# Performance work log

Hardware: AMD Instinct MI355X
Metric: run time of the kernel (lower is better)

Reference implementation:

```python
import jax, jax.numpy as jnp
import numpy as np

N_NODES = 100000
IN_DIM, HID_DIM, OUT_DIM = 1433, 16, 7
N_EDGES = 3200000


def gcn_conv(x, edge_index, W, b, num_nodes):
    # add self loops
    loop = jnp.arange(num_nodes, dtype=edge_index.dtype)
    src = jnp.concatenate([edge_index[0], loop])  # [E+N]
    dst = jnp.concatenate([edge_index[1], loop])
    h = x @ W + b  # [N, out]
    # degree computed on row (edge_index[0]) as in the torch code
    deg = jax.ops.segment_sum(jnp.ones_like(src, dtype=h.dtype), src,
                              num_segments=num_nodes)
    dis = deg ** -0.5  # self-loops guarantee deg >= 1
    norm = dis[src] * dis[dst]  # [E+N]
    msg = norm[:, None] * h[src]  # gather + scale
    return jax.ops.segment_sum(msg, dst, num_segments=num_nodes)  # scatter-add


def setup_inputs() -> dict:
    key = jax.random.key(0)
    k1, k2, k3, k4, k5, k6 = jax.random.split(key, 6)
    x = jax.random.normal(k1, (N_NODES, IN_DIM), dtype=jnp.float32)
    edge_index = jax.random.randint(k2, (2, N_EDGES), 0, N_NODES, dtype=jnp.int64)
    s1 = 1.0 / np.sqrt(IN_DIM)
    s2 = 1.0 / np.sqrt(HID_DIM)
    W1 = jax.random.uniform(k3, (IN_DIM, HID_DIM), jnp.float32, -s1, s1)
    b1 = jax.random.uniform(k4, (HID_DIM,), jnp.float32, -s1, s1)
    W2 = jax.random.uniform(k5, (HID_DIM, OUT_DIM), jnp.float32, -s2, s2)
    b2 = jax.random.uniform(k6, (OUT_DIM,), jnp.float32, -s2, s2)
    return {"x": x, "edge_index": edge_index, "W1": W1, "b1": b1,
            "W2": W2, "b2": b2}


def reference(x, edge_index, W1, b1, W2, b2):
    n = x.shape[0]
    h = gcn_conv(x, edge_index, W1, b1, n)
    h = jax.nn.relu(h)
    # dropout is inactive in eval mode (training=False)
    h = gcn_conv(h, edge_index, W2, b2, n)
    return jax.nn.log_softmax(h, axis=1)
```

## Files before the change

kernel.cpp:

```cpp
#include <hip/hip_runtime.h>
#include <math.h>

constexpr int IN_DIM = 1433;
constexpr int HID    = 16;
constexpr int OUTD   = 7;

__device__ __forceinline__ int edge_get(const int* __restrict__ ei, long long idx, int is64) {
    return is64 ? ei[2 * idx] : ei[idx];
}

__global__ void k_detect(const int* __restrict__ ei, int* __restrict__ flag) {
    __shared__ int nzsh;
    if (threadIdx.x == 0) nzsh = 0;
    __syncthreads();
    int nz = 0;
    for (int i = threadIdx.x; i < 2048; i += blockDim.x)
        nz |= (ei[2 * i + 1] != 0) ? 1 : 0;
    if (nz) nzsh = 1;
    __syncthreads();
    if (threadIdx.x == 0) *flag = (nzsh == 0) ? 1 : 0;
}

__global__ void k_init_new(int* __restrict__ deg, int* __restrict__ cnt, int n) {
    int i = blockIdx.x * blockDim.x + threadIdx.x;
    if (i < n) { deg[i] = 1; cnt[i] = 0; }
}

__global__ void k_deg_finish(float* __restrict__ dis, int n) {
    int i = blockIdx.x * blockDim.x + threadIdx.x;
    if (i < n) {
        int v = ((const int*)dis)[i];
        dis[i] = rsqrtf((float)v);
    }
}

__global__ __launch_bounds__(128) void k_gemm1h(
        const float* __restrict__ x, const float* __restrict__ W1,
        const float* __restrict__ b1, float* __restrict__ h1, int n,
        const int* __restrict__ ei, int E, const int* __restrict__ flag,
        int* __restrict__ deg, int* __restrict__ cnt, int nHist) {
    if ((int)blockIdx.x < nHist) {
        int is64 = *flag;
        long long stride = (long long)nHist * blockDim.x;
        for (long long e = (long long)blockIdx.x * blockDim.x + threadIdx.x;
             e < E; e += stride) {
            int s = edge_get(ei, e, is64);
            int d = edge_get(ei, (long long)E + e, is64);
            atomicAdd(&deg[s], 1);
            atomicAdd(&cnt[d], 1);
        }
        return;
    }

    constexpr int BK = 32, XST = 36;
    __shared__ __align__(16) float xs[128 * XST];
    __shared__ __align__(16) float wsm[BK * HID];
    const int t    = threadIdx.x;
    const int c4   = t & 3;
    const int rq   = t >> 2;
    const int row0 = ((int)blockIdx.x - nHist) * 128;

    float xreg[32];
    float wreg[4];
    float acc[16];
    #pragma unroll
    for (int j = 0; j < 16; ++j) acc[j] = 0.f;

    auto issue = [&](int kt) {
        #pragma unroll
        for (int i = 0; i < 32; ++i) {
            int idx  = t + 128 * i;
            int srow = idx >> 5;
            int scol = idx & 31;
            int gr   = row0 + srow;
            int col  = kt + scol;
            float v = 0.f;
            if (gr < n && col < IN_DIM) v = x[(long long)gr * IN_DIM + col];
            xreg[i] = v;
        }
        #pragma unroll
        for (int u = 0; u < 4; ++u) {
            int idx = t + 128 * u;
            int kk  = idx >> 4;
            wreg[u] = (kt + kk < IN_DIM) ? W1[(kt + kk) * HID + (idx & 15)] : 0.f;
        }
    };
    auto commit = [&]() {
        #pragma unroll
        for (int i = 0; i < 32; ++i) {
            int idx  = t + 128 * i;
            int srow = idx >> 5;
            int scol = idx & 31;
            xs[srow * XST + scol] = xreg[i];
        }
        #pragma unroll
        for (int u = 0; u < 4; ++u) wsm[t + 128 * u] = wreg[u];
    };

    const int nkt = (IN_DIM + BK - 1) / BK;
    issue(0);
    for (int it = 0; it < nkt; ++it) {
        commit();
        __syncthreads();
        if (it + 1 < nkt) issue((it + 1) * BK);
        #pragma unroll 8
        for (int k = 0; k < BK; ++k) {
            float4 w = *(const float4*)&wsm[k * HID + c4 * 4];
            #pragma unroll
            for (int j = 0; j < 4; ++j) {
                float xv = xs[(rq + 32 * j) * XST + k];
                acc[j * 4 + 0] += xv * w.x;
                acc[j * 4 + 1] += xv * w.y;
                acc[j * 4 + 2] += xv * w.z;
                acc[j * 4 + 3] += xv * w.w;
            }
        }
        __syncthreads();
    }

    float4 bv = *(const float4*)&b1[c4 * 4];
    #pragma unroll
    for (int j = 0; j < 4; ++j) {
        int gr = row0 + rq + 32 * j;
        if (gr < n) {
            float4 hv;
            hv.x = acc[j * 4 + 0] + bv.x;
            hv.y = acc[j * 4 + 1] + bv.y;
            hv.z = acc[j * 4 + 2] + bv.z;
            hv.w = acc[j * 4 + 3] + bv.w;
            *(float4*)&h1[(long long)gr * HID + c4 * 4] = hv;
        }
    }
}

__global__ void k_scale(const float* __restrict__ dis, const float* __restrict__ in,
                        float* __restrict__ out, int n, int squared) {
    int i = blockIdx.x * blockDim.x + threadIdx.x;
    if (i >= n * 4) return;
    int row = i >> 2;
    float d = dis[row];
    if (squared) d *= d;
    float4 v = *(const float4*)&in[(long long)i * 4];
    v.x *= d; v.y *= d; v.z *= d; v.w *= d;
    *(float4*)&out[(long long)i * 4] = v;
}

__global__ __launch_bounds__(256) void k_scan1(const int* __restrict__ cnt,
                                               int* __restrict__ bsum, int n) {
    __shared__ int sh[256];
    int t = threadIdx.x;
    int base = blockIdx.x * 1024 + t * 4;
    int s = 0;
    #pragma unroll
    for (int j = 0; j < 4; ++j) {
        int i = base + j;
        if (i < n) s += cnt[i];
    }
    sh[t] = s; __syncthreads();
    for (int o = 128; o > 0; o >>= 1) {
        if (t < o) sh[t] += sh[t + o];
        __syncthreads();
    }
    if (t == 0) bsum[blockIdx.x] = sh[0];
}

__global__ __launch_bounds__(256) void k_scan2(const int* __restrict__ bsum,
                                               int* __restrict__ boff,
                                               int* __restrict__ rp,
                                               int nb, int n, int E) {
    __shared__ int sh[256];
    int t = threadIdx.x;
    int v = (t < nb) ? bsum[t] : 0;
    sh[t] = v; __syncthreads();
    for (int o = 1; o < 256; o <<= 1) {
        int tmp = (t >= o) ? sh[t - o] : 0;
        __syncthreads();
        sh[t] += tmp;
        __syncthreads();
    }
    boff[t] = sh[t] - v;
    if (t == 0) rp[n] = E;
}

__global__ __launch_bounds__(256) void k_scan3(const int* __restrict__ cnt,
                                               const int* __restrict__ boff,
                                               int* __restrict__ rp,
                                               int* __restrict__ cur, int n) {
    __shared__ int sh[256];
    int t = threadIdx.x;
    int base = blockIdx.x * 1024 + t * 4;
    int c[4];
    int s = 0;
    #pragma unroll
    for (int j = 0; j < 4; ++j) {
        int i = base + j;
        c[j] = (i < n) ? cnt[i] : 0;
        s += c[j];
    }
    sh[t] = s; __syncthreads();
    for (int o = 1; o < 256; o <<= 1) {
        int tmp = (t >= o) ? sh[t - o] : 0;
        __syncthreads();
        sh[t] += tmp;
        __syncthreads();
    }
    int run = boff[blockIdx.x] + sh[t] - s;
    #pragma unroll
    for (int j = 0; j < 4; ++j) {
        int i = base + j;
        if (i < n) { rp[i] = run; cur[i] = run; }
        run += c[j];
    }
}

__global__ void k_fill(const int* __restrict__ ei, int E, const int* __restrict__ flag,
                       int* __restrict__ cur, int* __restrict__ csr) {
    int e = blockIdx.x * blockDim.x + threadIdx.x;
    if (e >= E) return;
    int is64 = *flag;
    int s = edge_get(ei, e, is64);
    int d = edge_get(ei, (long long)E + e, is64);
    int slot = atomicAdd(&cur[d], 1);
    csr[slot] = s;
}

__global__ __launch_bounds__(256) void k_gather1f(
        const int* __restrict__ rp, const int* __restrict__ csr,
        const float* __restrict__ dis, const float* __restrict__ hs1,
        const float* __restrict__ W2, const float* __restrict__ b2,
        float* __restrict__ hs2, int n) {
    __shared__ float w2s[HID * OUTD];
    __shared__ float b2s[OUTD];
    int t = threadIdx.x;
    if (t < HID * OUTD) w2s[t] = W2[t];
    if (t < OUTD) b2s[t] = b2[t];
    __syncthreads();

    int tid  = blockIdx.x * blockDim.x + t;
    int node = tid >> 2;
    int q    = tid & 3;
    if (node >= n) return;

    float4 acc = *(const float4*)&hs1[(long long)node * HID + q * 4];

    int i = rp[node], end = rp[node + 1];
    if (i < end) {
        int    s1  = csr[i];
        float4 hv1 = *(const float4*)&hs1[(long long)s1 * HID + q * 4];
        for (++i; i < end; ++i) {
            int    s2  = csr[i];
            float4 hv2 = *(const float4*)&hs1[(long long)s2 * HID + q * 4];
            acc.x += hv1.x; acc.y += hv1.y; acc.z += hv1.z; acc.w += hv1.w;
            hv1 = hv2;
        }
        acc.x += hv1.x; acc.y += hv1.y; acc.z += hv1.z; acc.w += hv1.w;
    }

    float dn = dis[node];
    float r0 = fmaxf(dn * acc.x, 0.f), r1 = fmaxf(dn * acc.y, 0.f);
    float r2 = fmaxf(dn * acc.z, 0.f), r3 = fmaxf(dn * acc.w, 0.f);
    float p[OUTD];
    #pragma unroll
    for (int j = 0; j < OUTD; ++j) {
        p[j] = r0 * w2s[(q * 4 + 0) * OUTD + j]
             + r1 * w2s[(q * 4 + 1) * OUTD + j]
             + r2 * w2s[(q * 4 + 2) * OUTD + j]
             + r3 * w2s[(q * 4 + 3) * OUTD + j];
    }
    #pragma unroll
    for (int j = 0; j < OUTD; ++j) {
        p[j] += __shfl_xor(p[j], 1, 4);
        p[j] += __shfl_xor(p[j], 2, 4);
    }
    hs2[(long long)node * OUTD + q] = dn * (p[q] + b2s[q]);
    if (q < 3) hs2[(long long)node * OUTD + q + 4] = dn * (p[q + 4] + b2s[q + 4]);
}

__global__ __launch_bounds__(256) void k_gather2(
        const int* __restrict__ rp, const int* __restrict__ csr,
        const float* __restrict__ dis, const float* __restrict__ hs2,
        float* __restrict__ out, int n) {
    int t = threadIdx.x;
    int node = blockIdx.x * 32 + (t >> 3);
    int q = t & 7;
    if (node >= n) return;
    float acc = -1e30f;
    if (q < OUTD) {
        acc = hs2[(long long)node * OUTD + q];
        int i = rp[node], end = rp[node + 1];
        if (i < end) {
            int   s1 = csr[i];
            float v1 = hs2[(long long)s1 * OUTD + q];
            for (++i; i < end; ++i) {
                int   s2 = csr[i];
                float v2 = hs2[(long long)s2 * OUTD + q];
                acc += v1;
                v1 = v2;
            }
            acc += v1;
        }
        acc *= dis[node];
    }
    float m = acc;
    #pragma unroll
    for (int o = 1; o < 8; o <<= 1) m = fmaxf(m, __shfl_xor(m, o, 8));
    float ex = (q < OUTD) ? expf(acc - m) : 0.f;
    float ss = ex;
    #pragma unroll
    for (int o = 1; o < 8; o <<= 1) ss += __shfl_xor(ss, o, 8);
    if (q < OUTD) out[(long long)node * OUTD + q] = acc - m - logf(ss);
}

__global__ void k_deg_init(int* __restrict__ deg, int n) {
    int i = blockIdx.x * blockDim.x + threadIdx.x;
    if (i < n) deg[i] = 1;
}

__global__ void k_deg_count(const int* __restrict__ ei, int E,
                            const int* __restrict__ flag, int* __restrict__ deg) {
    int e = blockIdx.x * blockDim.x + threadIdx.x;
    if (e >= E) return;
    int is64 = *flag;
    int s = edge_get(ei, e, is64);
    atomicAdd(&deg[s], 1);
}

__global__ void k_agg1(const int* __restrict__ ei, int E, const int* __restrict__ flag,
                       const float* __restrict__ dis, const float* __restrict__ h1,
                       float* __restrict__ a1) {
    long long tid = (long long)blockIdx.x * blockDim.x + threadIdx.x;
    int e = (int)(tid >> 2);
    int q = (int)(tid & 3);
    if (e >= E) return;
    int is64 = *flag;
    int s = edge_get(ei, e, is64);
    int d = edge_get(ei, (long long)E + e, is64);
    float nrm = dis[s] * dis[d];
    float4 v = *(const float4*)&h1[(long long)s * HID + q * 4];
    float* o = &a1[(long long)d * HID + q * 4];
    atomicAdd(o + 0, nrm * v.x);
    atomicAdd(o + 1, nrm * v.y);
    atomicAdd(o + 2, nrm * v.z);
    atomicAdd(o + 3, nrm * v.w);
}

__global__ __launch_bounds__(256) void k_gemm2(
        const float* __restrict__ a1, const float* __restrict__ W2,
        const float* __restrict__ b2, const float* __restrict__ dis,
        float* __restrict__ h2, float* __restrict__ a2, int n) {
    __shared__ float w2s[HID * OUTD];
    __shared__ float b2s[OUTD];
    int t = threadIdx.x;
    if (t < HID * OUTD) w2s[t] = W2[t];
    if (t < OUTD) b2s[t] = b2[t];
    __syncthreads();
    int r = blockIdx.x * blockDim.x + t;
    if (r >= n) return;
    float a[16];
    #pragma unroll
    for (int i = 0; i < 4; ++i) {
        float4 v = *(const float4*)&a1[(long long)r * HID + i * 4];
        a[4 * i + 0] = fmaxf(v.x, 0.f);
        a[4 * i + 1] = fmaxf(v.y, 0.f);
        a[4 * i + 2] = fmaxf(v.z, 0.f);
        a[4 * i + 3] = fmaxf(v.w, 0.f);
    }
    float dd = 0.f;
    if (a2) { float d = dis[r]; dd = d * d; }
    #pragma unroll
    for (int j = 0; j < OUTD; ++j) {
        float acc = b2s[j];
        #pragma unroll
        for (int k = 0; k < HID; ++k) acc += a[k] * w2s[k * OUTD + j];
        h2[(long long)r * OUTD + j] = acc;
        if (a2) a2[(long long)r * OUTD + j] = dd * acc;
    }
}

__global__ void k_agg2(const int* __restrict__ ei, int E, const int* __restrict__ flag,
                       const float* __restrict__ dis, const float* __restrict__ h2,
                       float* __restrict__ a2) {
    long long tid = (long long)blockIdx.x * blockDim.x + threadIdx.x;
    int e = (int)(tid >> 1);
    int q = (int)(tid & 1);
    if (e >= E) return;
    int is64 = *flag;
    int s = edge_get(ei, e, is64);
    int d = edge_get(ei, (long long)E + e, is64);
    float nrm = dis[s] * dis[d];
    int cnt = q ? 3 : 4;
    long long bs = (long long)s * OUTD + q * 4;
    long long bd = (long long)d * OUTD + q * 4;
    #pragma unroll
    for (int j = 0; j < 4; ++j)
        if (j < cnt) atomicAdd(&a2[bd + j], nrm * h2[bs + j]);
}

__global__ void k_lsm(const float* __restrict__ a2, float* __restrict__ out, int n) {
    int r = blockIdx.x * blockDim.x + threadIdx.x;
    if (r >= n) return;
    float v[OUTD];
    #pragma unroll
    for (int j = 0; j < OUTD; ++j) v[j] = a2[(long long)r * OUTD + j];
    float m = v[0];
    #pragma unroll
    for (int j = 1; j < OUTD; ++j) m = fmaxf(m, v[j]);
    float ssum = 0.f;
    #pragma unroll
    for (int j = 0; j < OUTD; ++j) ssum += expf(v[j] - m);
    float l = logf(ssum);
    #pragma unroll
    for (int j = 0; j < OUTD; ++j) out[(long long)r * OUTD + j] = v[j] - m - l;
}

extern "C" void kernel_launch(void* const* d_in, const int* in_sizes, int n_in,
                              void* d_out, int out_size, void* d_ws, size_t ws_size,
                              hipStream_t stream) {
    const float* x  = (const float*)d_in[0];
    const int*   ei = (const int*)d_in[1];
    const float* W1 = (const float*)d_in[2];
    const float* b1 = (const float*)d_in[3];
    const float* W2 = (const float*)d_in[4];
    const float* b2 = (const float*)d_in[5];
    float* out = (float*)d_out;

    const int N = in_sizes[0] / IN_DIM;
    const int E = in_sizes[1] / 2;

    const int TPB = 256;
    const int gN  = (N + TPB - 1) / TPB;
    const int gE  = (E + TPB - 1) / TPB;
    const int gG1 = (N + 127) / 128;
    const int NB  = (N + 1023) / 1024;
    const int nHist = 512;

    float* ws = (float*)d_ws;
    size_t o = 0;
    auto take = [&](size_t cnt) { size_t r = o; o += (cnt + 127) & ~(size_t)127; return r; };

    size_t off_dis  = take((size_t)N);
    size_t off_flag = take(64);
    size_t off_cnt  = take((size_t)N);
    size_t off_rp   = take((size_t)N + 1);
    size_t off_cur  = take((size_t)N);
    size_t off_bs   = take(256);
    size_t off_bo   = take(256);
    size_t off_csr  = take((size_t)E);
    size_t off_h1   = take((size_t)N * HID);
    size_t off_h2   = take((size_t)N * OUTD);
    size_t need_new = o * sizeof(float);

    if (ws_size >= need_new) {
        float* dis  = ws + off_dis;
        int*   degi = (int*)dis;
        int*   flag = (int*)(ws + off_flag);
        int*   cnt  = (int*)(ws + off_cnt);
        int*   rp   = (int*)(ws + off_rp);
        int*   cur  = (int*)(ws + off_cur);
        int*   bs   = (int*)(ws + off_bs);
        int*   bo   = (int*)(ws + off_bo);
        int*   csr  = (int*)(ws + off_csr);
        float* h1   = ws + off_h1;
        float* hs2  = ws + off_h2;

        k_detect<<<1, 256, 0, stream>>>(ei, flag);
        k_init_new<<<gN, TPB, 0, stream>>>(degi, cnt, N);
        k_gemm1h<<<nHist + gG1, 128, 0, stream>>>(x, W1, b1, h1, N,
                                                  ei, E, flag, degi, cnt, nHist);
        k_deg_finish<<<gN, TPB, 0, stream>>>(dis, N);
        k_scan1<<<NB, 256, 0, stream>>>(cnt, bs, N);
        k_scan2<<<1, 256, 0, stream>>>(bs, bo, rp, NB, N, E);
        k_scan3<<<NB, 256, 0, stream>>>(cnt, bo, rp, cur, N);
        k_scale<<<(int)(((long long)N * 4 + TPB - 1) / TPB), TPB, 0, stream>>>(
            dis, h1, h1, N, 0);
        k_fill<<<gE, TPB, 0, stream>>>(ei, E, flag, cur, csr);
        k_gather1f<<<(int)(((long long)N * 4 + TPB - 1) / TPB), TPB, 0, stream>>>(
            rp, csr, dis, h1, W2, b2, hs2, N);
        k_gather2<<<(N + 31) / 32, 256, 0, stream>>>(rp, csr, dis, hs2, out, N);
    } else {
        o = 0;
        size_t f_dis  = take((size_t)N);
        size_t f_flag = take(64);
        size_t f_h1   = take((size_t)N * HID);
        size_t f_a1   = take((size_t)N * HID);
        size_t f_h2   = take((size_t)N * OUTD);
        size_t f_a2   = take((size_t)N * OUTD);

        float* dis  = ws + f_dis;
        int*   degi = (int*)dis;
        int*   flag = (int*)(ws + f_flag);
        float* h1   = ws + f_h1;
        float* a1   = ws + f_a1;
        float* h2   = ws + f_h2;
        float* a2   = ws + f_a2;

        int g4E = (int)(((long long)4 * E + TPB - 1) / TPB);
        int g2E = (int)(((long long)2 * E + TPB - 1) / TPB);

        k_detect<<<1, 256, 0, stream>>>(ei, flag);
        k_deg_init<<<gN, TPB, 0, stream>>>(degi, N);
        k_deg_count<<<gE, TPB, 0, stream>>>(ei, E, flag, degi);
        k_deg_finish<<<gN, TPB, 0, stream>>>(dis, N);
        k_gemm1h<<<gG1, 128, 0, stream>>>(x, W1, b1, h1, N,
                                          ei, E, flag, nullptr, nullptr, 0);
        k_scale<<<(int)(((long long)N * 4 + TPB - 1) / TPB), TPB, 0, stream>>>(
            dis, h1, a1, N, 1);
        k_agg1<<<g4E, TPB, 0, stream>>>(ei, E, flag, dis, h1, a1);
        k_gemm2<<<gN, TPB, 0, stream>>>(a1, W2, b2, dis, h2, a2, N);
        k_agg2<<<g2E, TPB, 0, stream>>>(ei, E, flag, dis, h2, a2);
        k_lsm<<<gN, TPB, 0, stream>>>(a2, out, N);
    }
}
```

Measured before the change: 776.4 us.

## Split histogram from GEMM, record per-edge slots, and unroll gathers

```diff
diff --git a/kernel.cpp b/kernel.cpp
--- a/kernel.cpp
+++ b/kernel.cpp
@@ -34,37 +34,115 @@
     }
 }
 
-__global__ __launch_bounds__(128) void k_gemm1h(
+__global__ void k_hist2(const int* __restrict__ ei, int E, const int* __restrict__ flag,
+                        int* __restrict__ deg, int* __restrict__ cnt,
+                        int* __restrict__ packed) {
+    int e = blockIdx.x * blockDim.x + threadIdx.x;
+    if (e >= E) return;
+    int is64 = *flag;
+    int s = edge_get(ei, e, is64);
+    int d = edge_get(ei, (long long)E + e, is64);
+    atomicAdd(&deg[s], 1);
+    int slot = atomicAdd(&cnt[d], 1);
+    packed[e] = (d << 14) | (slot & 16383);
+}
+
+__global__ void k_place(const int* __restrict__ ei, int E, const int* __restrict__ flag,
+                        const int* __restrict__ packed, const int* __restrict__ rp,
+                        int* __restrict__ csr) {
+    int e = blockIdx.x * blockDim.x + threadIdx.x;
+    if (e >= E) return;
+    int is64 = *flag;
+    int s  = edge_get(ei, e, is64);
+    int p  = packed[e];
+    int d  = p >> 14;
+    int sl = p & 16383;
+    csr[rp[d] + sl] = s;
+}
+
+__global__ __launch_bounds__(256) void k_scan1(const int* __restrict__ cnt,
+                                               int* __restrict__ bsum, int n) {
+    __shared__ int sh[256];
+    int t = threadIdx.x;
+    int base = blockIdx.x * 1024 + t * 4;
+    int s = 0;
+    #pragma unroll
+    for (int j = 0; j < 4; ++j) {
+        int i = base + j;
+        if (i < n) s += cnt[i];
+    }
+    sh[t] = s; __syncthreads();
+    for (int o = 128; o > 0; o >>= 1) {
+        if (t < o) sh[t] += sh[t + o];
+        __syncthreads();
+    }
+    if (t == 0) bsum[blockIdx.x] = sh[0];
+}
+
+__global__ __launch_bounds__(256) void k_scan2(const int* __restrict__ bsum,
+                                               int* __restrict__ boff,
+                                               int* __restrict__ rp,
+                                               int nb, int n, int E) {
+    __shared__ int sh[256];
+    int t = threadIdx.x;
+    int v = (t < nb) ? bsum[t] : 0;
+    sh[t] = v; __syncthreads();
+    for (int o = 1; o < 256; o <<= 1) {
+        int tmp = (t >= o) ? sh[t - o] : 0;
+        __syncthreads();
+        sh[t] += tmp;
+        __syncthreads();
+    }
+    boff[t] = sh[t] - v;
+    if (t == 0) rp[n] = E;
+}
+
+__global__ __launch_bounds__(256) void k_scan3(const int* __restrict__ cnt,
+                                               const int* __restrict__ boff,
+                                               int* __restrict__ rp, int n) {
+    __shared__ int sh[256];
+    int t = threadIdx.x;
+    int base = blockIdx.x * 1024 + t * 4;
+    int c[4];
+    int s = 0;
+    #pragma unroll
+    for (int j = 0; j < 4; ++j) {
+        int i = base + j;
+        c[j] = (i < n) ? cnt[i] : 0;
+        s += c[j];
+    }
+    sh[t] = s; __syncthreads();
+    for (int o = 1; o < 256; o <<= 1) {
+        int tmp = (t >= o) ? sh[t - o] : 0;
+        __syncthreads();
+        sh[t] += tmp;
+        __syncthreads();
+    }
+    int run = boff[blockIdx.x] + sh[t] - s;
+    #pragma unroll
+    for (int j = 0; j < 4; ++j) {
+        int i = base + j;
+        if (i < n) rp[i] = run;
+        run += c[j];
+    }
+}
+
+__global__ __launch_bounds__(128) void k_gemm1(
         const float* __restrict__ x, const float* __restrict__ W1,
-        const float* __restrict__ b1, float* __restrict__ h1, int n,
-        const int* __restrict__ ei, int E, const int* __restrict__ flag,
-        int* __restrict__ deg, int* __restrict__ cnt, int nHist) {
-    if ((int)blockIdx.x < nHist) {
-        int is64 = *flag;
-        long long stride = (long long)nHist * blockDim.x;
-        for (long long e = (long long)blockIdx.x * blockDim.x + threadIdx.x;
-             e < E; e += stride) {
-            int s = edge_get(ei, e, is64);
-            int d = edge_get(ei, (long long)E + e, is64);
-            atomicAdd(&deg[s], 1);
-            atomicAdd(&cnt[d], 1);
-        }
-        return;
-    }
-
+        const float* __restrict__ b1, float* __restrict__ h1, int n) {
     constexpr int BK = 32, XST = 36;
     __shared__ __align__(16) float xs[128 * XST];
     __shared__ __align__(16) float wsm[BK * HID];
     const int t    = threadIdx.x;
     const int c4   = t & 3;
     const int rq   = t >> 2;
-    const int row0 = ((int)blockIdx.x - nHist) * 128;
+    const int row0 = blockIdx.x * 128;
 
     float xreg[32];
     float wreg[4];
-    float acc[16];
-    #pragma unroll
-    for (int j = 0; j < 16; ++j) acc[j] = 0.f;
+    float4 acc[4];
+    #pragma unroll
+    for (int j = 0; j < 4; ++j) acc[j] = make_float4(0.f, 0.f, 0.f, 0.f);
 
     auto issue = [&](int kt) {
         #pragma unroll
@@ -103,16 +181,20 @@
         commit();
         __syncthreads();
         if (it + 1 < nkt) issue((it + 1) * BK);
-        #pragma unroll 8
-        for (int k = 0; k < BK; ++k) {
-            float4 w = *(const float4*)&wsm[k * HID + c4 * 4];
+        #pragma unroll
+        for (int k4 = 0; k4 < BK / 4; ++k4) {
+            int k = k4 * 4;
+            float4 w0 = *(const float4*)&wsm[(k + 0) * HID + c4 * 4];
+            float4 w1 = *(const float4*)&wsm[(k + 1) * HID + c4 * 4];
+            float4 w2 = *(const float4*)&wsm[(k + 2) * HID + c4 * 4];
+            float4 w3 = *(const float4*)&wsm[(k + 3) * HID + c4 * 4];
             #pragma unroll
             for (int j = 0; j < 4; ++j) {
-                float xv = xs[(rq + 32 * j) * XST + k];
-                acc[j * 4 + 0] += xv * w.x;
-                acc[j * 4 + 1] += xv * w.y;
-                acc[j * 4 + 2] += xv * w.z;
-                acc[j * 4 + 3] += xv * w.w;
+                float4 xv = *(const float4*)&xs[(rq + 32 * j) * XST + k];
+                acc[j].x += xv.x * w0.x + xv.y * w1.x + xv.z * w2.x + xv.w * w3.x;
+                acc[j].y += xv.x * w0.y + xv.y * w1.y + xv.z * w2.y + xv.w * w3.y;
+                acc[j].z += xv.x * w0.z + xv.y * w1.z + xv.z * w2.z + xv.w * w3.z;
+                acc[j].w += xv.x * w0.w + xv.y * w1.w + xv.z * w2.w + xv.w * w3.w;
             }
         }
         __syncthreads();
@@ -124,10 +206,10 @@
         int gr = row0 + rq + 32 * j;
         if (gr < n) {
             float4 hv;
-            hv.x = acc[j * 4 + 0] + bv.x;
-            hv.y = acc[j * 4 + 1] + bv.y;
-            hv.z = acc[j * 4 + 2] + bv.z;
-            hv.w = acc[j * 4 + 3] + bv.w;
+            hv.x = acc[j].x + bv.x;
+            hv.y = acc[j].y + bv.y;
+            hv.z = acc[j].z + bv.z;
+            hv.w = acc[j].w + bv.w;
             *(float4*)&h1[(long long)gr * HID + c4 * 4] = hv;
         }
     }
@@ -143,85 +225,6 @@
     float4 v = *(const float4*)&in[(long long)i * 4];
     v.x *= d; v.y *= d; v.z *= d; v.w *= d;
     *(float4*)&out[(long long)i * 4] = v;
-}
-
-__global__ __launch_bounds__(256) void k_scan1(const int* __restrict__ cnt,
-                                               int* __restrict__ bsum, int n) {
-    __shared__ int sh[256];
-    int t = threadIdx.x;
-    int base = blockIdx.x * 1024 + t * 4;
-    int s = 0;
-    #pragma unroll
-    for (int j = 0; j < 4; ++j) {
-        int i = base + j;
-        if (i < n) s += cnt[i];
-    }
-    sh[t] = s; __syncthreads();
-    for (int o = 128; o > 0; o >>= 1) {
-        if (t < o) sh[t] += sh[t + o];
-        __syncthreads();
-    }
-    if (t == 0) bsum[blockIdx.x] = sh[0];
-}
-
-__global__ __launch_bounds__(256) void k_scan2(const int* __restrict__ bsum,
-                                               int* __restrict__ boff,
-                                               int* __restrict__ rp,
-                                               int nb, int n, int E) {
-    __shared__ int sh[256];
-    int t = threadIdx.x;
-    int v = (t < nb) ? bsum[t] : 0;
-    sh[t] = v; __syncthreads();
-    for (int o = 1; o < 256; o <<= 1) {
-        int tmp = (t >= o) ? sh[t - o] : 0;
-        __syncthreads();
-        sh[t] += tmp;
-        __syncthreads();
-    }
-    boff[t] = sh[t] - v;
-    if (t == 0) rp[n] = E;
-}
-
-__global__ __launch_bounds__(256) void k_scan3(const int* __restrict__ cnt,
-                                               const int* __restrict__ boff,
-                                               int* __restrict__ rp,
-                                               int* __restrict__ cur, int n) {
-    __shared__ int sh[256];
-    int t = threadIdx.x;
-    int base = blockIdx.x * 1024 + t * 4;
-    int c[4];
-    int s = 0;
-    #pragma unroll
-    for (int j = 0; j < 4; ++j) {
-        int i = base + j;
-        c[j] = (i < n) ? cnt[i] : 0;
-        s += c[j];
-    }
-    sh[t] = s; __syncthreads();
-    for (int o = 1; o < 256; o <<= 1) {
-        int tmp = (t >= o) ? sh[t - o] : 0;
-        __syncthreads();
-        sh[t] += tmp;
-        __syncthreads();
-    }
-    int run = boff[blockIdx.x] + sh[t] - s;
-    #pragma unroll
-    for (int j = 0; j < 4; ++j) {
-        int i = base + j;
-        if (i < n) { rp[i] = run; cur[i] = run; }
-        run += c[j];
-    }
-}
-
-__global__ void k_fill(const int* __restrict__ ei, int E, const int* __restrict__ flag,
-                       int* __restrict__ cur, int* __restrict__ csr) {
-    int e = blockIdx.x * blockDim.x + threadIdx.x;
-    if (e >= E) return;
-    int is64 = *flag;
-    int s = edge_get(ei, e, is64);
-    int d = edge_get(ei, (long long)E + e, is64);
-    int slot = atomicAdd(&cur[d], 1);
-    csr[slot] = s;
 }
 
 __global__ __launch_bounds__(256) void k_gather1f(
@@ -244,16 +247,21 @@
     float4 acc = *(const float4*)&hs1[(long long)node * HID + q * 4];
 
     int i = rp[node], end = rp[node + 1];
-    if (i < end) {
-        int    s1  = csr[i];
-        float4 hv1 = *(const float4*)&hs1[(long long)s1 * HID + q * 4];
-        for (++i; i < end; ++i) {
-            int    s2  = csr[i];
-            float4 hv2 = *(const float4*)&hs1[(long long)s2 * HID + q * 4];
-            acc.x += hv1.x; acc.y += hv1.y; acc.z += hv1.z; acc.w += hv1.w;
-            hv1 = hv2;
-        }
-        acc.x += hv1.x; acc.y += hv1.y; acc.z += hv1.z; acc.w += hv1.w;
+    for (; i + 4 <= end; i += 4) {
+        int s0 = csr[i], s1 = csr[i + 1], s2 = csr[i + 2], s3 = csr[i + 3];
+        float4 h0 = *(const float4*)&hs1[(long long)s0 * HID + q * 4];
+        float4 h1 = *(const float4*)&hs1[(long long)s1 * HID + q * 4];
+        float4 h2 = *(const float4*)&hs1[(long long)s2 * HID + q * 4];
+        float4 h3 = *(const float4*)&hs1[(long long)s3 * HID + q * 4];
+        acc.x += (h0.x + h1.x) + (h2.x + h3.x);
+        acc.y += (h0.y + h1.y) + (h2.y + h3.y);
+        acc.z += (h0.z + h1.z) + (h2.z + h3.z);
+        acc.w += (h0.w + h1.w) + (h2.w + h3.w);
+    }
+    for (; i < end; ++i) {
+        int s = csr[i];
+        float4 h = *(const float4*)&hs1[(long long)s * HID + q * 4];
+        acc.x += h.x; acc.y += h.y; acc.z += h.z; acc.w += h.w;
     }
 
     float dn = dis[node];
@@ -288,16 +296,22 @@
     if (q < OUTD) {
         acc = hs2[(long long)node * OUTD + q];
         int i = rp[node], end = rp[node + 1];
-        if (i < end) {
-            int   s1 = csr[i];
+        for (; i + 8 <= end; i += 8) {
+            int s0 = csr[i],     s1 = csr[i + 1], s2 = csr[i + 2], s3 = csr[i + 3];
+            int s4 = csr[i + 4], s5 = csr[i + 5], s6 = csr[i + 6], s7 = csr[i + 7];
+            float v0 = hs2[(long long)s0 * OUTD + q];
             float v1 = hs2[(long long)s1 * OUTD + q];
-            for (++i; i < end; ++i) {
-                int   s2 = csr[i];
-                float v2 = hs2[(long long)s2 * OUTD + q];
-                acc += v1;
-                v1 = v2;
-            }
-            acc += v1;
+            float v2 = hs2[(long long)s2 * OUTD + q];
+            float v3 = hs2[(long long)s3 * OUTD + q];
+            float v4 = hs2[(long long)s4 * OUTD + q];
+            float v5 = hs2[(long long)s5 * OUTD + q];
+            float v6 = hs2[(long long)s6 * OUTD + q];
+            float v7 = hs2[(long long)s7 * OUTD + q];
+            acc += ((v0 + v1) + (v2 + v3)) + ((v4 + v5) + (v6 + v7));
+        }
+        for (; i < end; ++i) {
+            int s = csr[i];
+            acc += hs2[(long long)s * OUTD + q];
         }
         acc *= dis[node];
     }
@@ -432,7 +446,6 @@
     const int gE  = (E + TPB - 1) / TPB;
     const int gG1 = (N + 127) / 128;
     const int NB  = (N + 1023) / 1024;
-    const int nHist = 512;
 
     float* ws = (float*)d_ws;
     size_t o = 0;
@@ -442,9 +455,9 @@
     size_t off_flag = take(64);
     size_t off_cnt  = take((size_t)N);
     size_t off_rp   = take((size_t)N + 1);
-    size_t off_cur  = take((size_t)N);
     size_t off_bs   = take(256);
     size_t off_bo   = take(256);
+    size_t off_pk   = take((size_t)E);
     size_t off_csr  = take((size_t)E);
     size_t off_h1   = take((size_t)N * HID);
     size_t off_h2   = take((size_t)N * OUTD);
@@ -456,24 +469,24 @@
         int*   flag = (int*)(ws + off_flag);
         int*   cnt  = (int*)(ws + off_cnt);
         int*   rp   = (int*)(ws + off_rp);
-        int*   cur  = (int*)(ws + off_cur);
         int*   bs   = (int*)(ws + off_bs);
         int*   bo   = (int*)(ws + off_bo);
+        int*   pk   = (int*)(ws + off_pk);
         int*   csr  = (int*)(ws + off_csr);
         float* h1   = ws + off_h1;
         float* hs2  = ws + off_h2;
 
         k_detect<<<1, 256, 0, stream>>>(ei, flag);
         k_init_new<<<gN, TPB, 0, stream>>>(degi, cnt, N);
-        k_gemm1h<<<nHist + gG1, 128, 0, stream>>>(x, W1, b1, h1, N,
-                                                  ei, E, flag, degi, cnt, nHist);
+        k_hist2<<<gE, TPB, 0, stream>>>(ei, E, flag, degi, cnt, pk);
         k_deg_finish<<<gN, TPB, 0, stream>>>(dis, N);
         k_scan1<<<NB, 256, 0, stream>>>(cnt, bs, N);
         k_scan2<<<1, 256, 0, stream>>>(bs, bo, rp, NB, N, E);
-        k_scan3<<<NB, 256, 0, stream>>>(cnt, bo, rp, cur, N);
+        k_scan3<<<NB, 256, 0, stream>>>(cnt, bo, rp, N);
+        k_place<<<gE, TPB, 0, stream>>>(ei, E, flag, pk, rp, csr);
+        k_gemm1<<<gG1, 128, 0, stream>>>(x, W1, b1, h1, N);
         k_scale<<<(int)(((long long)N * 4 + TPB - 1) / TPB), TPB, 0, stream>>>(
             dis, h1, h1, N, 0);
-        k_fill<<<gE, TPB, 0, stream>>>(ei, E, flag, cur, csr);
         k_gather1f<<<(int)(((long long)N * 4 + TPB - 1) / TPB), TPB, 0, stream>>>(
             rp, csr, dis, h1, W2, b2, hs2, N);
         k_gather2<<<(N + 31) / 32, 256, 0, stream>>>(rp, csr, dis, hs2, out, N);
@@ -501,8 +514,7 @@
         k_deg_init<<<gN, TPB, 0, stream>>>(degi, N);
         k_deg_count<<<gE, TPB, 0, stream>>>(ei, E, flag, degi);
         k_deg_finish<<<gN, TPB, 0, stream>>>(dis, N);
-        k_gemm1h<<<gG1, 128, 0, stream>>>(x, W1, b1, h1, N,
-                                          ei, E, flag, nullptr, nullptr, 0);
+        k_gemm1<<<gG1, 128, 0, stream>>>(x, W1, b1, h1, N);
         k_scale<<<(int)(((long long)N * 4 + TPB - 1) / TPB), TPB, 0, stream>>>(
             dis, h1, a1, N, 1);
         k_agg1<<<g4E, TPB, 0, stream>>>(ei, E, flag, dis, h1, a1);
```

Measured after the change: 633.1 us. 1.23x faster.
